# Kernel optimization log

Measured on AMD Instinct MI355X. Metric: run time of the kernel, lower is better.

## Reference

```python
import jax, jax.numpy as jnp
import numpy as np
import math

N_EMBD = 1024
N_HEAD = 16
BLOCK_SIZE = 2048
B, T = 2, 2048


def setup_inputs() -> dict:
    key = jax.random.key(0)
    ks = jax.random.split(key, 12)
    s = 0.02
    C = N_EMBD
    return {
        "x": jax.random.normal(ks[0], (B, T, C), dtype=jnp.float32),
        # LayerNorm 1
        "ln1_w": jnp.ones((C,), jnp.float32),
        "ln1_b": jnp.zeros((C,), jnp.float32),
        # attention: weights stored [in, out]
        "attn_w": jax.random.normal(ks[1], (C, 3 * C), dtype=jnp.float32) * s,
        "attn_b": jnp.zeros((3 * C,), jnp.float32),
        "proj_w": jax.random.normal(ks[2], (C, C), dtype=jnp.float32) * s,
        "proj_b": jnp.zeros((C,), jnp.float32),
        # LayerNorm 2
        "ln2_w": jnp.ones((C,), jnp.float32),
        "ln2_b": jnp.zeros((C,), jnp.float32),
        # MLP
        "fc_w": jax.random.normal(ks[3], (C, 4 * C), dtype=jnp.float32) * s,
        "fc_b": jnp.zeros((4 * C,), jnp.float32),
        "mlp_proj_w": jax.random.normal(ks[4], (4 * C, C), dtype=jnp.float32) * s,
        "mlp_proj_b": jnp.zeros((C,), jnp.float32),
    }


def _layernorm(x, w, b, eps=1e-5):
    mu = jnp.mean(x, axis=-1, keepdims=True)
    var = jnp.mean(jnp.square(x - mu), axis=-1, keepdims=True)
    return (x - mu) * jax.lax.rsqrt(var + eps) * w + b


def _attention(x, attn_w, attn_b, proj_w, proj_b):
    Bn, Tn, C = x.shape
    hs = C // N_HEAD
    qkv = x @ attn_w + attn_b                      # [B,T,3C]
    q, k, v = jnp.split(qkv, 3, axis=-1)
    # [B,H,T,hs]
    q = q.reshape(Bn, Tn, N_HEAD, hs).transpose(0, 2, 1, 3)
    k = k.reshape(Bn, Tn, N_HEAD, hs).transpose(0, 2, 1, 3)
    v = v.reshape(Bn, Tn, N_HEAD, hs).transpose(0, 2, 1, 3)
    att = jnp.einsum('bhqd,bhkd->bhqk', q, k) / math.sqrt(hs)  # [B,H,T,T]
    mask = jnp.tril(jnp.ones((Tn, Tn), dtype=bool))
    att = jnp.where(mask, att, -jnp.inf)
    att = jax.nn.softmax(att, axis=-1)
    y = jnp.einsum('bhqk,bhkd->bhqd', att, v)      # [B,H,T,hs]
    y = y.transpose(0, 2, 1, 3).reshape(Bn, Tn, C)
    return y @ proj_w + proj_b


def reference(x, ln1_w, ln1_b, attn_w, attn_b, proj_w, proj_b,
              ln2_w, ln2_b, fc_w, fc_b, mlp_proj_w, mlp_proj_b):
    x = x + _attention(_layernorm(x, ln1_w, ln1_b), attn_w, attn_b, proj_w, proj_b)
    h = _layernorm(x, ln2_w, ln2_b)
    h = jax.nn.gelu(h @ fc_w + fc_b, approximate=False)  # torch nn.GELU default = exact erf
    return x + (h @ mlp_proj_w + mlp_proj_b)
```

## Files before the change

kernel.cpp:

```cpp
#include <hip/hip_runtime.h>
#include <math.h>

typedef short s8x __attribute__((ext_vector_type(8)));
typedef float f32x4 __attribute__((ext_vector_type(4)));

__device__ __forceinline__ float bf2f(short u) {
    return __uint_as_float(((unsigned int)(unsigned short)u) << 16);
}
__device__ __forceinline__ short f2bf(float f) {
    unsigned int x = __float_as_uint(f);
    unsigned int r = (x + 0x7FFFu + ((x >> 16) & 1u)) >> 16;
    return (short)(unsigned short)r;
}
__device__ __forceinline__ short f2bf_trunc(float f) {
    return (short)(__float_as_uint(f) >> 16);
}

__device__ __forceinline__ void gl2lds16(const short* g, const short* l) {
    __builtin_amdgcn_global_load_lds(
        (const __attribute__((address_space(1))) void*)(unsigned long long)g,
        (__attribute__((address_space(3))) void*)(unsigned int)(unsigned long long)l,
        16, 0, 0);
}

__device__ __forceinline__ void ln_row(const float* __restrict__ xin,
                                       const float* __restrict__ w,
                                       const float* __restrict__ bb,
                                       short* __restrict__ out, int row, int lane) {
    const float4* xr = (const float4*)(xin + (long)row * 1024);
    float4 v[4];
    float s1 = 0.f, s2 = 0.f;
#pragma unroll
    for (int i = 0; i < 4; ++i) {
        v[i] = xr[lane + i * 64];
        s1 += v[i].x + v[i].y + v[i].z + v[i].w;
        s2 += v[i].x*v[i].x + v[i].y*v[i].y + v[i].z*v[i].z + v[i].w*v[i].w;
    }
#pragma unroll
    for (int off = 32; off > 0; off >>= 1) {
        s1 += __shfl_xor(s1, off, 64);
        s2 += __shfl_xor(s2, off, 64);
    }
    const float mu = s1 * (1.0f / 1024.0f);
    float var = s2 * (1.0f / 1024.0f) - mu * mu;
    var = fmaxf(var, 0.0f);
    const float rs = rsqrtf(var + 1e-5f);
    short4* orow = (short4*)(out + (long)row * 1024);
#pragma unroll
    for (int i = 0; i < 4; ++i) {
        const int ci = (lane + i * 64) * 4;
        const float4 wv = *(const float4*)(w + ci);
        const float4 bv = *(const float4*)(bb + ci);
        short4 o;
        o.x = f2bf((v[i].x - mu) * rs * wv.x + bv.x);
        o.y = f2bf((v[i].y - mu) * rs * wv.y + bv.y);
        o.z = f2bf((v[i].z - mu) * rs * wv.z + bv.z);
        o.w = f2bf((v[i].w - mu) * rs * wv.w + bv.w);
        orow[lane + i * 64] = o;
    }
}

__global__ __launch_bounds__(256) void ln_k(const float* __restrict__ xin,
                                            const float* __restrict__ w,
                                            const float* __restrict__ bb,
                                            short* __restrict__ out) {
    ln_row(xin, w, bb, out, blockIdx.x * 4 + (threadIdx.x >> 6), threadIdx.x & 63);
}

__global__ __launch_bounds__(256) void pre_k(
        const float* __restrict__ w0, const float* __restrict__ w1,
        const float* __restrict__ w2, const float* __restrict__ w3,
        short* __restrict__ o0, short* __restrict__ o1,
        short* __restrict__ o2, short* __restrict__ o3,
        const float* __restrict__ x, const float* __restrict__ ln1w,
        const float* __restrict__ ln1b, short* __restrict__ xln) {
    int bid = blockIdx.x;
    if (bid >= 12288) {
        ln_row(x, ln1w, ln1b, xln, (bid - 12288) * 4 + (threadIdx.x >> 6), threadIdx.x & 63);
        return;
    }
    const float* in; short* out; int K, N, nx;
    if (bid < 3072)      { in = w0; out = o0; K = 1024; N = 3072; nx = 96; }
    else if (bid < 4096) { bid -= 3072; in = w1; out = o1; K = 1024; N = 1024; nx = 32; }
    else if (bid < 8192) { bid -= 4096; in = w2; out = o2; K = 1024; N = 4096; nx = 128; }
    else                 { bid -= 8192; in = w3; out = o3; K = 4096; N = 1024; nx = 32; }
    const int n0 = (bid % nx) * 32, k0 = (bid / nx) * 32;
    __shared__ float tile[32][33];
    const int tx = threadIdx.x & 31, ty = threadIdx.x >> 5;
#pragma unroll
    for (int i = 0; i < 4; ++i) {
        const int k = ty + i * 8;
        tile[k][tx] = in[(long)(k0 + k) * N + n0 + tx];
    }
    __syncthreads();
#pragma unroll
    for (int i = 0; i < 4; ++i) {
        const int n = ty + i * 8;
        out[(long)(n0 + n) * K + k0 + tx] = f2bf(tile[tx][n]);
    }
}

template <int EPI, typename OutT>
__device__ __forceinline__ void epi_store(OutT* out, const float* resid, long oidx, float v) {
    if constexpr (EPI == 0) {
        out[oidx] = f2bf(v);
    } else if constexpr (EPI == 1) {
        const float u = v * (0.79788456080f + 0.03567740814f * v * v);
        v = v / (1.0f + __expf(-2.0f * u));
        out[oidx] = f2bf(v);
    } else {
        v += resid[oidx];
        out[oidx] = v;
    }
}

template <int EPI, typename OutT>
__global__ __launch_bounds__(256) void gemm_k(const short* __restrict__ A,
                                              const short* __restrict__ Bt,
                                              const float* __restrict__ bias,
                                              const float* __restrict__ resid,
                                              OutT* __restrict__ out,
                                              int M, int N, int K) {
    __shared__ __align__(16) short sA[2][128 * 32];
    __shared__ __align__(16) short sB[2][128 * 32];
    const int tid = threadIdx.x;
    const int lane = tid & 63, wave = tid >> 6;
    const int wr = (wave >> 1) * 64, wc = (wave & 1) * 64;
    const int lrow = lane & 15, quad = lane >> 4;
    const int bm = blockIdx.y * 128, bn = blockIdx.x * 128;
    const short* Ap = A + (long)(bm + (tid >> 2)) * K + (tid & 3) * 8;
    const short* Bp = Bt + (long)(bn + (tid >> 2)) * K + (tid & 3) * 8;
    const long rowstep = (long)64 * K;

    auto stage = [&](int p, int k0) {
        gl2lds16(Ap + k0,           sA[p] + tid * 8);
        gl2lds16(Ap + rowstep + k0, sA[p] + 2048 + tid * 8);
        gl2lds16(Bp + k0,           sB[p] + tid * 8);
        gl2lds16(Bp + rowstep + k0, sB[p] + 2048 + tid * 8);
    };

    f32x4 acc[4][4] = {};
    stage(0, 0);
    const int S = K >> 5;
    for (int s = 0; s < S; ++s) {
        const int p = s & 1;
        __syncthreads();
        if (s + 1 < S) stage(p ^ 1, (s + 1) << 5);
        const short* pA = sA[p];
        const short* pB = sB[p];
        s8x af[4], bfr[4];
#pragma unroll
        for (int i = 0; i < 4; ++i) af[i]  = *(const s8x*)(pA + (wr + i*16 + lrow) * 32 + quad * 8);
#pragma unroll
        for (int j = 0; j < 4; ++j) bfr[j] = *(const s8x*)(pB + (wc + j*16 + lrow) * 32 + quad * 8);
#pragma unroll
        for (int i = 0; i < 4; ++i)
#pragma unroll
            for (int j = 0; j < 4; ++j)
                acc[i][j] = __builtin_amdgcn_mfma_f32_16x16x32_bf16(af[i], bfr[j], acc[i][j], 0, 0, 0);
    }
#pragma unroll
    for (int i = 0; i < 4; ++i) {
#pragma unroll
        for (int j = 0; j < 4; ++j) {
#pragma unroll
            for (int r = 0; r < 4; ++r) {
                const int row = bm + wr + i*16 + quad*4 + r;
                const int col = bn + wc + j*16 + lrow;
                epi_store<EPI>(out, resid, (long)row * N + col, acc[i][j][r] + bias[col]);
            }
        }
    }
}

template <int EPI, typename OutT>
__global__ __launch_bounds__(256) void gemm64_k(const short* __restrict__ A,
                                                const short* __restrict__ Bt,
                                                const float* __restrict__ bias,
                                                const float* __restrict__ resid,
                                                OutT* __restrict__ out,
                                                int M, int N, int K) {
    __shared__ __align__(16) short sA[2][2][64 * 32];
    __shared__ __align__(16) short sB[2][2][128 * 32];
    const int tid = threadIdx.x;
    const int lane = tid & 63, wave = tid >> 6;
    const int lrow = lane & 15, quad = lane >> 4;
    const int bm = blockIdx.y * 64, bn = blockIdx.x * 128;
    const short* Ap = A + (long)(bm + (tid >> 2)) * K + (tid & 3) * 8;
    const short* Bp = Bt + (long)(bn + (tid >> 2)) * K + (tid & 3) * 8;
    const long rowstep = (long)64 * K;

    auto stage = [&](int p, int k0) {
#pragma unroll
        for (int hp = 0; hp < 2; ++hp) {
            gl2lds16(Ap + k0 + hp * 32,           sA[p][hp] + tid * 8);
            gl2lds16(Bp + k0 + hp * 32,           sB[p][hp] + tid * 8);
            gl2lds16(Bp + rowstep + k0 + hp * 32, sB[p][hp] + 2048 + tid * 8);
        }
    };

    f32x4 acc[8] = {};
    stage(0, 0);
    const int S = K >> 6;
    for (int s = 0; s < S; ++s) {
        const int p = s & 1;
        __syncthreads();
        if (s + 1 < S) stage(p ^ 1, (s + 1) << 6);
#pragma unroll
        for (int hp = 0; hp < 2; ++hp) {
            const s8x af = *(const s8x*)(sA[p][hp] + (wave * 16 + lrow) * 32 + quad * 8);
#pragma unroll
            for (int j = 0; j < 8; ++j) {
                const s8x bf = *(const s8x*)(sB[p][hp] + (j * 16 + lrow) * 32 + quad * 8);
                acc[j] = __builtin_amdgcn_mfma_f32_16x16x32_bf16(af, bf, acc[j], 0, 0, 0);
            }
        }
    }
#pragma unroll
    for (int j = 0; j < 8; ++j) {
#pragma unroll
        for (int r = 0; r < 4; ++r) {
            const int row = bm + wave * 16 + quad * 4 + r;
            const int col = bn + j * 16 + lrow;
            epi_store<EPI>(out, resid, (long)row * N + col, acc[j][r] + bias[col]);
        }
    }
}

#define ATT_CS (0.125f * 1.4426950408889634f)
#define ATT_C0 (14.426950408889634f)

__global__ __launch_bounds__(256) void attn_k(const short* __restrict__ qkv,
                                              short* __restrict__ y) {
    const int bx = blockIdx.x;
    const int b = blockIdx.y >> 4, h = blockIdx.y & 15;
    const int qtA = bx, qtB = 31 - bx;
    const int tid = threadIdx.x, lane = tid & 63, wave = tid >> 6;
    const int lrow = lane & 15, quad = lane >> 4;
    const long base = (long)b * 2048 * 3072;

    __shared__ __align__(16) short sK[2][64 * 64];
    __shared__ __align__(16) short sVt[2][64 * 64];
    __shared__ __align__(16) short sP[64 * 72];

    s8x qfA0, qfA1, qfB0, qfB1;
    {
        const short* qpA = qkv + base + (long)(qtA * 64 + wave * 16 + lrow) * 3072 + h * 64 + quad * 8;
        qfA0 = *(const s8x*)qpA; qfA1 = *(const s8x*)(qpA + 32);
        const short* qpB = qkv + base + (long)(qtB * 64 + wave * 16 + lrow) * 3072 + h * 64 + quad * 8;
        qfB0 = *(const s8x*)qpB; qfB1 = *(const s8x*)(qpB + 32);
    }
    f32x4 oA[4], oB[4], lA = {}, lB = {};
#pragma unroll
    for (int d = 0; d < 4; ++d) { oA[d] = f32x4{0.f,0.f,0.f,0.f}; oB[d] = f32x4{0.f,0.f,0.f,0.f}; }
    s8x ones;
#pragma unroll
    for (int j = 0; j < 8; ++j) ones[j] = (short)0x3F80;

    const int srow = tid >> 3, sg = tid & 7;
    const int sw0 = ((srow & 7) ^ (srow >> 3)) & 7;
    const int sw1 = (((srow + 32) & 7) ^ ((srow + 32) >> 3)) & 7;
    const short* kbase = qkv + base + 1024 + h * 64;
    const short* vbase = qkv + base + 2048 + h * 64;

    uint4 vr0, vr1;
    auto issueK = [&](int p, int k0) {
        gl2lds16(kbase + (long)(k0 + srow) * 3072      + (sg ^ sw0) * 8, sK[p] + tid * 8);
        gl2lds16(kbase + (long)(k0 + srow + 32) * 3072 + (sg ^ sw1) * 8, sK[p] + 2048 + tid * 8);
    };
    auto loadV = [&](int k0) {
        const short* vp = vbase + (long)(k0 + srow) * 3072 + sg * 8;
        vr0 = *(const uint4*)vp;
        vr1 = *(const uint4*)(vp + 32 * 3072);
    };
    auto writeV = [&](int p) {
        const short* e0 = (const short*)&vr0;
        const short* e1 = (const short*)&vr1;
#pragma unroll
        for (int i = 0; i < 8; ++i) {
            const int d = sg * 8 + i;
            const int swd = i ^ sg;
            sVt[p][d * 64 + ( srow       ^ (swd << 3))] = e0[i];
            sVt[p][d * 64 + ((srow + 32) ^ (swd << 3))] = e1[i];
        }
    };

    auto tile_step = [&](const s8x& qf0, const s8x& qf1, const s8x* kf0, const s8x* kf1,
                         const short* pV, f32x4* o, f32x4& lacc, int qt, int kt, int k0) {
        f32x4 s[4];
#pragma unroll
        for (int ct = 0; ct < 4; ++ct) {
            f32x4 t = f32x4{0.f, 0.f, 0.f, 0.f};
            t = __builtin_amdgcn_mfma_f32_16x16x32_bf16(qf0, kf0[ct], t, 0, 0, 0);
            t = __builtin_amdgcn_mfma_f32_16x16x32_bf16(qf1, kf1[ct], t, 0, 0, 0);
            s[ct] = t;
        }
        if (kt == qt) {
            const int qrow = qt * 64 + wave * 16 + quad * 4;
#pragma unroll
            for (int ct = 0; ct < 4; ++ct) {
                const int key = k0 + ct * 16 + lrow;
#pragma unroll
                for (int r = 0; r < 4; ++r) {
                    const float e = (key > qrow + r) ? -1e30f : fmaf(s[ct][r], ATT_CS, -ATT_C0);
                    s[ct][r] = exp2f(e);
                }
            }
        } else {
#pragma unroll
            for (int ct = 0; ct < 4; ++ct)
#pragma unroll
                for (int r = 0; r < 4; ++r)
                    s[ct][r] = exp2f(fmaf(s[ct][r], ATT_CS, -ATT_C0));
        }
#pragma unroll
        for (int ct = 0; ct < 4; ++ct)
#pragma unroll
            for (int r = 0; r < 4; ++r)
                sP[(wave * 16 + quad * 4 + r) * 72 + ct * 16 + lrow] = f2bf_trunc(s[ct][r]);
#pragma unroll
        for (int ks = 0; ks < 2; ++ks) {
            const s8x pf = *(const s8x*)(sP + (wave * 16 + lrow) * 72 + ks * 32 + quad * 8);
            lacc = __builtin_amdgcn_mfma_f32_16x16x32_bf16(pf, ones, lacc, 0, 0, 0);
#pragma unroll
            for (int dt = 0; dt < 4; ++dt) {
                const int d = dt * 16 + lrow;
                const int swd = ((d & 7) ^ (d >> 3)) & 7;
                const s8x vf = *(const s8x*)(pV + d * 64 + (((ks * 4 + quad) ^ swd) * 8));
                o[dt] = __builtin_amdgcn_mfma_f32_16x16x32_bf16(pf, vf, o[dt], 0, 0, 0);
            }
        }
    };

    issueK(0, 0);
    loadV(0);
    for (int kt = 0; kt <= qtB; ++kt) {
        const int p = kt & 1, k0 = kt * 64;
        writeV(p);
        __syncthreads();
        if (kt < qtB) { issueK(p ^ 1, k0 + 64); loadV(k0 + 64); }

        s8x kf0[4], kf1[4];
#pragma unroll
        for (int ct = 0; ct < 4; ++ct) {
            const int row = ct * 16 + lrow;
            const int swr = ((row & 7) ^ (row >> 3)) & 7;
            kf0[ct] = *(const s8x*)(sK[p] + row * 64 + ((quad ^ swr) * 8));
            kf1[ct] = *(const s8x*)(sK[p] + row * 64 + (((4 + quad) ^ swr) * 8));
        }
        if (kt <= qtA) tile_step(qfA0, qfA1, kf0, kf1, sVt[p], oA, lA, qtA, kt, k0);
        tile_step(qfB0, qfB1, kf0, kf1, sVt[p], oB, lB, qtB, kt, k0);
    }
    float rA[4], rB[4];
#pragma unroll
    for (int r = 0; r < 4; ++r) { rA[r] = 1.0f / lA[r]; rB[r] = 1.0f / lB[r]; }
#pragma unroll
    for (int dt = 0; dt < 4; ++dt) {
#pragma unroll
        for (int r = 0; r < 4; ++r) {
            const int qA = qtA * 64 + wave * 16 + quad * 4 + r;
            const int qB = qtB * 64 + wave * 16 + quad * 4 + r;
            y[((long)b * 2048 + qA) * 1024 + h * 64 + dt * 16 + lrow] = f2bf(oA[dt][r] * rA[r]);
            y[((long)b * 2048 + qB) * 1024 + h * 64 + dt * 16 + lrow] = f2bf(oB[dt][r] * rB[r]);
        }
    }
}

extern "C" void kernel_launch(void* const* d_in, const int* in_sizes, int n_in,
                              void* d_out, int out_size, void* d_ws, size_t ws_size,
                              hipStream_t stream) {
    const float* x      = (const float*)d_in[0];
    const float* ln1_w  = (const float*)d_in[1];
    const float* ln1_b  = (const float*)d_in[2];
    const float* attn_w = (const float*)d_in[3];
    const float* attn_b = (const float*)d_in[4];
    const float* proj_w = (const float*)d_in[5];
    const float* proj_b = (const float*)d_in[6];
    const float* ln2_w  = (const float*)d_in[7];
    const float* ln2_b  = (const float*)d_in[8];
    const float* fc_w   = (const float*)d_in[9];
    const float* fc_b   = (const float*)d_in[10];
    const float* mlp_w  = (const float*)d_in[11];
    const float* mlp_b  = (const float*)d_in[12];

    char* ws = (char*)d_ws;
    short* attn_wt = (short*)(ws + 0);
    short* proj_wt = (short*)(ws + 6291456L);
    short* fc_wt   = (short*)(ws + 8388608L);
    short* mlp_wt  = (short*)(ws + 16777216L);
    short* slotA   = (short*)(ws + 25165824L);
    short* slotB   = (short*)(ws + 33554432L);

    short* xln  = slotA;
    short* yb   = slotA;
    short* hb   = slotA;
    short* qkvb = slotB;
    short* hh   = slotB;
    float* x1   = (float*)d_out;
    float* outp = (float*)d_out;

    pre_k<<<13312, 256, 0, stream>>>(attn_w, proj_w, fc_w, mlp_w,
                                     attn_wt, proj_wt, fc_wt, mlp_wt,
                                     x, ln1_w, ln1_b, xln);

    gemm_k<0, short><<<dim3(24, 32), 256, 0, stream>>>(xln, attn_wt, attn_b, nullptr, qkvb, 4096, 3072, 1024);
    attn_k<<<dim3(16, 32), 256, 0, stream>>>(qkvb, yb);
    gemm64_k<2, float><<<dim3(8, 64), 256, 0, stream>>>(yb, proj_wt, proj_b, x, x1, 4096, 1024, 1024);
    ln_k<<<1024, 256, 0, stream>>>(x1, ln2_w, ln2_b, hb);
    gemm_k<1, short><<<dim3(32, 32), 256, 0, stream>>>(hb, fc_wt, fc_b, nullptr, hh, 4096, 4096, 1024);
    gemm64_k<3, float><<<dim3(8, 64), 256, 0, stream>>>(hh, mlp_wt, mlp_b, x1, outp, 4096, 1024, 4096);
}
```

Measured before the change: 341.6 us.

## Rework attention kernel around 32x32 MFMA with register-resident P via permlane swap

Each workgroup now owns one 128-row query block instead of a pair of 64-row tiles, and launches the heaviest blocks first. Each wave handles 32 query rows and computes S^T with 32x32x16 bf16 MFMAs, taking K as the A operand. The probabilities are packed to bf16 and redistributed between lanes with permlane32_swap, so they feed the PV MFMA directly and never pass through LDS. The row sum is accumulated in registers instead of through an extra MFMA against a ones vector, and key chunks that are fully masked are skipped per wave; setprio hints are added around the MFMA runs. The risks are load imbalance, since blocks now carry unequal causal work, and higher register pressure from the 32x32 accumulators.

After: 365.6 us. 7.0% more time.

```diff
diff --git a/kernel.cpp b/kernel.cpp
--- a/kernel.cpp
+++ b/kernel.cpp
@@ -3,6 +3,7 @@
 
 typedef short s8x __attribute__((ext_vector_type(8)));
 typedef float f32x4 __attribute__((ext_vector_type(4)));
+typedef float f32x16 __attribute__((ext_vector_type(16)));
 
 __device__ __forceinline__ float bf2f(short u) {
     return __uint_as_float(((unsigned int)(unsigned short)u) << 16);
@@ -11,9 +12,6 @@
     unsigned int x = __float_as_uint(f);
     unsigned int r = (x + 0x7FFFu + ((x >> 16) & 1u)) >> 16;
     return (short)(unsigned short)r;
-}
-__device__ __forceinline__ short f2bf_trunc(float f) {
-    return (short)(__float_as_uint(f) >> 16);
 }
 
 __device__ __forceinline__ void gl2lds16(const short* g, const short* l) {
@@ -232,30 +230,28 @@
 
 __global__ __launch_bounds__(256) void attn_k(const short* __restrict__ qkv,
                                               short* __restrict__ y) {
-    const int bx = blockIdx.x;
+    const int j = 15 - (int)blockIdx.x;
     const int b = blockIdx.y >> 4, h = blockIdx.y & 15;
-    const int qtA = bx, qtB = 31 - bx;
     const int tid = threadIdx.x, lane = tid & 63, wave = tid >> 6;
-    const int lrow = lane & 15, quad = lane >> 4;
+    const int lq = lane & 31, hl = lane >> 5;
     const long base = (long)b * 2048 * 3072;
+    const int qb0 = j * 128;
+    const int qrow = qb0 + wave * 32 + lq;
+    const int ktlast = 2 * j + 1;
+    const int qmin_w = qb0 + wave * 32, qmax_w = qmin_w + 31;
 
     __shared__ __align__(16) short sK[2][64 * 64];
     __shared__ __align__(16) short sVt[2][64 * 64];
-    __shared__ __align__(16) short sP[64 * 72];
-
-    s8x qfA0, qfA1, qfB0, qfB1;
+    __shared__ float sL[128];
+
+    s8x qf[4];
     {
-        const short* qpA = qkv + base + (long)(qtA * 64 + wave * 16 + lrow) * 3072 + h * 64 + quad * 8;
-        qfA0 = *(const s8x*)qpA; qfA1 = *(const s8x*)(qpA + 32);
-        const short* qpB = qkv + base + (long)(qtB * 64 + wave * 16 + lrow) * 3072 + h * 64 + quad * 8;
-        qfB0 = *(const s8x*)qpB; qfB1 = *(const s8x*)(qpB + 32);
-    }
-    f32x4 oA[4], oB[4], lA = {}, lB = {};
-#pragma unroll
-    for (int d = 0; d < 4; ++d) { oA[d] = f32x4{0.f,0.f,0.f,0.f}; oB[d] = f32x4{0.f,0.f,0.f,0.f}; }
-    s8x ones;
-#pragma unroll
-    for (int j = 0; j < 8; ++j) ones[j] = (short)0x3F80;
+        const short* qp = qkv + base + (long)qrow * 3072 + h * 64 + hl * 8;
+#pragma unroll
+        for (int c = 0; c < 4; ++c) qf[c] = *(const s8x*)(qp + c * 16);
+    }
+    f32x16 acc[2] = {};
+    float lsum = 0.f;
 
     const int srow = tid >> 3, sg = tid & 7;
     const int sw0 = ((srow & 7) ^ (srow >> 3)) & 7;
@@ -285,83 +281,99 @@
         }
     };
 
-    auto tile_step = [&](const s8x& qf0, const s8x& qf1, const s8x* kf0, const s8x* kf1,
-                         const short* pV, f32x4* o, f32x4& lacc, int qt, int kt, int k0) {
-        f32x4 s[4];
-#pragma unroll
-        for (int ct = 0; ct < 4; ++ct) {
-            f32x4 t = f32x4{0.f, 0.f, 0.f, 0.f};
-            t = __builtin_amdgcn_mfma_f32_16x16x32_bf16(qf0, kf0[ct], t, 0, 0, 0);
-            t = __builtin_amdgcn_mfma_f32_16x16x32_bf16(qf1, kf1[ct], t, 0, 0, 0);
-            s[ct] = t;
-        }
-        if (kt == qt) {
-            const int qrow = qt * 64 + wave * 16 + quad * 4;
-#pragma unroll
-            for (int ct = 0; ct < 4; ++ct) {
-                const int key = k0 + ct * 16 + lrow;
-#pragma unroll
-                for (int r = 0; r < 4; ++r) {
-                    const float e = (key > qrow + r) ? -1e30f : fmaf(s[ct][r], ATT_CS, -ATT_C0);
-                    s[ct][r] = exp2f(e);
-                }
-            }
-        } else {
-#pragma unroll
-            for (int ct = 0; ct < 4; ++ct)
-#pragma unroll
-                for (int r = 0; r < 4; ++r)
-                    s[ct][r] = exp2f(fmaf(s[ct][r], ATT_CS, -ATT_C0));
-        }
-#pragma unroll
-        for (int ct = 0; ct < 4; ++ct)
-#pragma unroll
-            for (int r = 0; r < 4; ++r)
-                sP[(wave * 16 + quad * 4 + r) * 72 + ct * 16 + lrow] = f2bf_trunc(s[ct][r]);
-#pragma unroll
-        for (int ks = 0; ks < 2; ++ks) {
-            const s8x pf = *(const s8x*)(sP + (wave * 16 + lrow) * 72 + ks * 32 + quad * 8);
-            lacc = __builtin_amdgcn_mfma_f32_16x16x32_bf16(pf, ones, lacc, 0, 0, 0);
-#pragma unroll
-            for (int dt = 0; dt < 4; ++dt) {
-                const int d = dt * 16 + lrow;
-                const int swd = ((d & 7) ^ (d >> 3)) & 7;
-                const s8x vf = *(const s8x*)(pV + d * 64 + (((ks * 4 + quad) ^ swd) * 8));
-                o[dt] = __builtin_amdgcn_mfma_f32_16x16x32_bf16(pf, vf, o[dt], 0, 0, 0);
-            }
-        }
-    };
-
-    issueK(0, 0);
-    loadV(0);
-    for (int kt = 0; kt <= qtB; ++kt) {
+    issueK(0, 0); loadV(0);
+    for (int kt = 0; kt <= ktlast; ++kt) {
         const int p = kt & 1, k0 = kt * 64;
         writeV(p);
         __syncthreads();
-        if (kt < qtB) { issueK(p ^ 1, k0 + 64); loadV(k0 + 64); }
-
-        s8x kf0[4], kf1[4];
-#pragma unroll
-        for (int ct = 0; ct < 4; ++ct) {
-            const int row = ct * 16 + lrow;
-            const int swr = ((row & 7) ^ (row >> 3)) & 7;
-            kf0[ct] = *(const s8x*)(sK[p] + row * 64 + ((quad ^ swr) * 8));
-            kf1[ct] = *(const s8x*)(sK[p] + row * 64 + (((4 + quad) ^ swr) * 8));
-        }
-        if (kt <= qtA) tile_step(qfA0, qfA1, kf0, kf1, sVt[p], oA, lA, qtA, kt, k0);
-        tile_step(qfB0, qfB1, kf0, kf1, sVt[p], oB, lB, qtB, kt, k0);
-    }
-    float rA[4], rB[4];
-#pragma unroll
-    for (int r = 0; r < 4; ++r) { rA[r] = 1.0f / lA[r]; rB[r] = 1.0f / lB[r]; }
-#pragma unroll
-    for (int dt = 0; dt < 4; ++dt) {
-#pragma unroll
-        for (int r = 0; r < 4; ++r) {
-            const int qA = qtA * 64 + wave * 16 + quad * 4 + r;
-            const int qB = qtB * 64 + wave * 16 + quad * 4 + r;
-            y[((long)b * 2048 + qA) * 1024 + h * 64 + dt * 16 + lrow] = f2bf(oA[dt][r] * rA[r]);
-            y[((long)b * 2048 + qB) * 1024 + h * 64 + dt * 16 + lrow] = f2bf(oB[dt][r] * rB[r]);
+        if (kt < ktlast) { issueK(p ^ 1, k0 + 64); loadV(k0 + 64); }
+#pragma unroll
+        for (int kc = 0; kc < 2; ++kc) {
+            const int kb0 = k0 + kc * 32;
+            if (kb0 > qmax_w) continue;
+
+            f32x16 st = {};
+            {
+                const int krow = kc * 32 + lq;
+                const int swr = ((krow & 7) ^ (krow >> 3)) & 7;
+                const short* kr = sK[p] + krow * 64;
+                s8x kf[4];
+#pragma unroll
+                for (int c = 0; c < 4; ++c)
+                    kf[c] = *(const s8x*)(kr + (((2 * c + hl) ^ swr) * 8));
+                __builtin_amdgcn_s_setprio(1);
+#pragma unroll
+                for (int c = 0; c < 4; ++c)
+                    st = __builtin_amdgcn_mfma_f32_32x32x16_bf16(kf[c], qf[c], st, 0, 0, 0);
+                __builtin_amdgcn_s_setprio(0);
+            }
+
+            const bool needmask = (kb0 + 31 > qmin_w);
+            float pv[16];
+            if (needmask) {
+#pragma unroll
+                for (int r = 0; r < 16; ++r) {
+                    const int key = kb0 + (r & 3) + 8 * (r >> 2) + 4 * hl;
+                    const float pp = exp2f(fmaf(st[r], ATT_CS, -ATT_C0));
+                    const float pt = __uint_as_float(__float_as_uint(pp) & 0xFFFF0000u);
+                    pv[r] = (key > qrow) ? 0.f : pt;
+                }
+            } else {
+#pragma unroll
+                for (int r = 0; r < 16; ++r) {
+                    const float pp = exp2f(fmaf(st[r], ATT_CS, -ATT_C0));
+                    pv[r] = __uint_as_float(__float_as_uint(pp) & 0xFFFF0000u);
+                }
+            }
+            lsum += (((pv[0] + pv[1]) + (pv[2] + pv[3])) + ((pv[4] + pv[5]) + (pv[6] + pv[7])))
+                  + (((pv[8] + pv[9]) + (pv[10] + pv[11])) + ((pv[12] + pv[13]) + (pv[14] + pv[15])));
+
+            unsigned int w[8];
+#pragma unroll
+            for (int t = 0; t < 8; ++t)
+                w[t] = __builtin_amdgcn_perm(__float_as_uint(pv[2 * t + 1]),
+                                             __float_as_uint(pv[2 * t]), 0x07060302u);
+            s8x pa[2];
+#pragma unroll
+            for (int s = 0; s < 2; ++s) {
+                auto r02 = __builtin_amdgcn_permlane32_swap((int)w[4 * s + 0], (int)w[4 * s + 2], false, false);
+                auto r13 = __builtin_amdgcn_permlane32_swap((int)w[4 * s + 1], (int)w[4 * s + 3], false, false);
+                int4 f;
+                f.x = r02[0]; f.y = r13[0]; f.z = r02[1]; f.w = r13[1];
+                pa[s] = *(const s8x*)&f;
+            }
+
+            __builtin_amdgcn_s_setprio(1);
+#pragma unroll
+            for (int s = 0; s < 2; ++s) {
+#pragma unroll
+                for (int dt = 0; dt < 2; ++dt) {
+                    const int d = dt * 32 + lq;
+                    const int swd = ((d & 7) ^ (d >> 3)) & 7;
+                    const s8x vb = *(const s8x*)(sVt[p] + d * 64 + (((kc * 4 + s * 2 + hl) ^ swd) * 8));
+                    acc[dt] = __builtin_amdgcn_mfma_f32_32x32x16_bf16(pa[s], vb, acc[dt], 0, 0, 0);
+                }
+            }
+            __builtin_amdgcn_s_setprio(0);
+        }
+    }
+
+    lsum += __shfl_xor(lsum, 32, 64);
+    if (lane < 32) sL[wave * 32 + lq] = 1.0f / lsum;
+    float rinv[16];
+#pragma unroll
+    for (int rg = 0; rg < 4; ++rg) {
+        const float4 lv = *(const float4*)(sL + wave * 32 + rg * 8 + hl * 4);
+        rinv[rg * 4 + 0] = lv.x; rinv[rg * 4 + 1] = lv.y;
+        rinv[rg * 4 + 2] = lv.z; rinv[rg * 4 + 3] = lv.w;
+    }
+    const long ybase = ((long)b * 2048 + qb0 + wave * 32) * 1024 + h * 64;
+#pragma unroll
+    for (int dt = 0; dt < 2; ++dt) {
+#pragma unroll
+        for (int r = 0; r < 16; ++r) {
+            const int qloc = (r & 3) + 8 * (r >> 2) + 4 * hl;
+            y[ybase + (long)qloc * 1024 + dt * 32 + lq] = f2bf(acc[dt][r] * rinv[r]);
         }
     }
 }
```

## Keep attention probabilities in registers via transposed QK^T and permlane swaps

Applied to the files above, without the earlier changes.

Swaps the MFMA operand order so S^T is produced, which lets each lane build the P operand for the PV MFMA directly in registers using perm and permlane32/16 swaps. This removes the shared-memory round trip through sP. The row sum moves from an MFMA against a vector of ones to scalar adds plus end-of-kernel shuffles. It also adds s_setprio around the MFMA blocks, and relies on gfx950 permlane swap intrinsics and a correct lane mapping.

Result: no change. 343.6 us (+0.6%).

```diff
diff --git a/kernel.cpp b/kernel.cpp
--- a/kernel.cpp
+++ b/kernel.cpp
@@ -11,9 +11,6 @@
     unsigned int x = __float_as_uint(f);
     unsigned int r = (x + 0x7FFFu + ((x >> 16) & 1u)) >> 16;
     return (short)(unsigned short)r;
-}
-__device__ __forceinline__ short f2bf_trunc(float f) {
-    return (short)(__float_as_uint(f) >> 16);
 }
 
 __device__ __forceinline__ void gl2lds16(const short* g, const short* l) {
@@ -241,7 +238,6 @@
 
     __shared__ __align__(16) short sK[2][64 * 64];
     __shared__ __align__(16) short sVt[2][64 * 64];
-    __shared__ __align__(16) short sP[64 * 72];
 
     s8x qfA0, qfA1, qfB0, qfB1;
     {
@@ -250,12 +246,10 @@
         const short* qpB = qkv + base + (long)(qtB * 64 + wave * 16 + lrow) * 3072 + h * 64 + quad * 8;
         qfB0 = *(const s8x*)qpB; qfB1 = *(const s8x*)(qpB + 32);
     }
-    f32x4 oA[4], oB[4], lA = {}, lB = {};
+    f32x4 oA[4], oB[4];
+    float lA = 0.f, lB = 0.f;
 #pragma unroll
     for (int d = 0; d < 4; ++d) { oA[d] = f32x4{0.f,0.f,0.f,0.f}; oB[d] = f32x4{0.f,0.f,0.f,0.f}; }
-    s8x ones;
-#pragma unroll
-    for (int j = 0; j < 8; ++j) ones[j] = (short)0x3F80;
 
     const int srow = tid >> 3, sg = tid & 7;
     const int sw0 = ((srow & 7) ^ (srow >> 3)) & 7;
@@ -286,50 +280,72 @@
     };
 
     auto tile_step = [&](const s8x& qf0, const s8x& qf1, const s8x* kf0, const s8x* kf1,
-                         const short* pV, f32x4* o, f32x4& lacc, int qt, int kt, int k0) {
+                         const short* pV, f32x4* o, float& lsum, int qt, int kt, int k0) {
         f32x4 s[4];
+        __builtin_amdgcn_s_setprio(1);
 #pragma unroll
         for (int ct = 0; ct < 4; ++ct) {
             f32x4 t = f32x4{0.f, 0.f, 0.f, 0.f};
-            t = __builtin_amdgcn_mfma_f32_16x16x32_bf16(qf0, kf0[ct], t, 0, 0, 0);
-            t = __builtin_amdgcn_mfma_f32_16x16x32_bf16(qf1, kf1[ct], t, 0, 0, 0);
+            t = __builtin_amdgcn_mfma_f32_16x16x32_bf16(kf0[ct], qf0, t, 0, 0, 0);
+            t = __builtin_amdgcn_mfma_f32_16x16x32_bf16(kf1[ct], qf1, t, 0, 0, 0);
             s[ct] = t;
         }
+        __builtin_amdgcn_s_setprio(0);
+        const int qrow = qt * 64 + wave * 16 + lrow;
+        float pv[4][4];
         if (kt == qt) {
-            const int qrow = qt * 64 + wave * 16 + quad * 4;
-#pragma unroll
-            for (int ct = 0; ct < 4; ++ct) {
-                const int key = k0 + ct * 16 + lrow;
+#pragma unroll
+            for (int ct = 0; ct < 4; ++ct)
 #pragma unroll
                 for (int r = 0; r < 4; ++r) {
-                    const float e = (key > qrow + r) ? -1e30f : fmaf(s[ct][r], ATT_CS, -ATT_C0);
-                    s[ct][r] = exp2f(e);
+                    const int key = k0 + ct * 16 + quad * 4 + r;
+                    const float pp = exp2f(fmaf(s[ct][r], ATT_CS, -ATT_C0));
+                    const float pt = __uint_as_float(__float_as_uint(pp) & 0xFFFF0000u);
+                    pv[ct][r] = (key > qrow) ? 0.f : pt;
                 }
-            }
         } else {
 #pragma unroll
             for (int ct = 0; ct < 4; ++ct)
 #pragma unroll
-                for (int r = 0; r < 4; ++r)
-                    s[ct][r] = exp2f(fmaf(s[ct][r], ATT_CS, -ATT_C0));
+                for (int r = 0; r < 4; ++r) {
+                    const float pp = exp2f(fmaf(s[ct][r], ATT_CS, -ATT_C0));
+                    pv[ct][r] = __uint_as_float(__float_as_uint(pp) & 0xFFFF0000u);
+                }
         }
 #pragma unroll
         for (int ct = 0; ct < 4; ++ct)
-#pragma unroll
-            for (int r = 0; r < 4; ++r)
-                sP[(wave * 16 + quad * 4 + r) * 72 + ct * 16 + lrow] = f2bf_trunc(s[ct][r]);
+            lsum += (pv[ct][0] + pv[ct][1]) + (pv[ct][2] + pv[ct][3]);
+
+        unsigned int w2[4][2];
+#pragma unroll
+        for (int ct = 0; ct < 4; ++ct)
+#pragma unroll
+            for (int p2 = 0; p2 < 2; ++p2)
+                w2[ct][p2] = __builtin_amdgcn_perm(__float_as_uint(pv[ct][2 * p2 + 1]),
+                                                   __float_as_uint(pv[ct][2 * p2]), 0x07060302u);
+        s8x pa[2];
 #pragma unroll
         for (int ks = 0; ks < 2; ++ks) {
-            const s8x pf = *(const s8x*)(sP + (wave * 16 + lrow) * 72 + ks * 32 + quad * 8);
-            lacc = __builtin_amdgcn_mfma_f32_16x16x32_bf16(pf, ones, lacc, 0, 0, 0);
+            auto rAC = __builtin_amdgcn_permlane32_swap((int)w2[2 * ks][0], (int)w2[2 * ks + 1][0], false, false);
+            auto rBD = __builtin_amdgcn_permlane32_swap((int)w2[2 * ks][1], (int)w2[2 * ks + 1][1], false, false);
+            auto mAC = __builtin_amdgcn_permlane16_swap(rAC[0], rAC[1], false, false);
+            auto mBD = __builtin_amdgcn_permlane16_swap(rBD[0], rBD[1], false, false);
+            int4 f;
+            f.x = mAC[0]; f.y = mBD[0]; f.z = mAC[1]; f.w = mBD[1];
+            pa[ks] = *(const s8x*)&f;
+        }
+        __builtin_amdgcn_s_setprio(1);
+#pragma unroll
+        for (int ks = 0; ks < 2; ++ks) {
 #pragma unroll
             for (int dt = 0; dt < 4; ++dt) {
                 const int d = dt * 16 + lrow;
                 const int swd = ((d & 7) ^ (d >> 3)) & 7;
                 const s8x vf = *(const s8x*)(pV + d * 64 + (((ks * 4 + quad) ^ swd) * 8));
-                o[dt] = __builtin_amdgcn_mfma_f32_16x16x32_bf16(pf, vf, o[dt], 0, 0, 0);
+                o[dt] = __builtin_amdgcn_mfma_f32_16x16x32_bf16(pa[ks], vf, o[dt], 0, 0, 0);
             }
         }
+        __builtin_amdgcn_s_setprio(0);
     };
 
     issueK(0, 0);
@@ -351,9 +367,15 @@
         if (kt <= qtA) tile_step(qfA0, qfA1, kf0, kf1, sVt[p], oA, lA, qtA, kt, k0);
         tile_step(qfB0, qfB1, kf0, kf1, sVt[p], oB, lB, qtB, kt, k0);
     }
+
+    lA += __shfl_xor(lA, 16, 64); lA += __shfl_xor(lA, 32, 64);
+    lB += __shfl_xor(lB, 16, 64); lB += __shfl_xor(lB, 32, 64);
     float rA[4], rB[4];
 #pragma unroll
-    for (int r = 0; r < 4; ++r) { rA[r] = 1.0f / lA[r]; rB[r] = 1.0f / lB[r]; }
+    for (int r = 0; r < 4; ++r) {
+        rA[r] = 1.0f / __shfl(lA, quad * 4 + r, 64);
+        rB[r] = 1.0f / __shfl(lB, quad * 4 + r, 64);
+    }
 #pragma unroll
     for (int dt = 0; dt < 4; ++dt) {
 #pragma unroll
```
